# Kernel tuning notes

Measured on AMD Instinct MI355X. Metric: run time of the kernel, lower is better.

The kernel has to match this reference:

```python
import jax, jax.numpy as jnp
import numpy as np

HPC = 42  # HPC_FEATURES_LEN

def setup_inputs() -> dict:
    key = jax.random.key(0)
    ks = jax.random.split(key, 8)
    B, N, C, P, S = 4, 16384, 103, 2048, 32
    xyz = jax.random.normal(ks[0], (B, N, 3), dtype=jnp.float32)
    features = jax.random.normal(ks[1], (B, C, N), dtype=jnp.float32)
    new_xyz = jax.random.normal(ks[2], (B, P, 3), dtype=jnp.float32)
    idx = jax.random.randint(ks[3], (B, P, S), 0, N, dtype=jnp.int32)
    # 1x1-conv weights (out_ch, in_ch); gate conv sees full 3+C=106 channels
    Wg = jax.random.normal(ks[4], (64, 106), dtype=jnp.float32) * 0.05
    bg = jnp.zeros((64,), dtype=jnp.float32)
    W1 = jax.random.normal(ks[5], (64, 64), dtype=jnp.float32) * 0.05
    b1 = jnp.zeros((64,), dtype=jnp.float32)
    W2 = jax.random.normal(ks[6], (128, 64), dtype=jnp.float32) * 0.05
    b2 = jnp.zeros((128,), dtype=jnp.float32)
    W3 = jax.random.normal(ks[7], (256, 128), dtype=jnp.float32) * 0.05
    b3 = jnp.zeros((256,), dtype=jnp.float32)
    return {"xyz": xyz, "features": features, "new_xyz": new_xyz, "idx": idx,
            "Wg": Wg, "bg": bg, "W1": W1, "b1": b1, "W2": W2, "b2": b2,
            "W3": W3, "b3": b3}

def reference(xyz, features, new_xyz, idx, Wg, bg, W1, b1, W2, b2, W3, b3):
    # --- grouping: gather neighbors, center xyz, concat features ---
    # grouped_xyz: (B, P, S, 3) -> (B, 3, P, S)
    grouped_xyz = jax.vmap(lambda x, i: x[i])(xyz, idx) - new_xyz[:, :, None, :]
    grouped_xyz = jnp.transpose(grouped_xyz, (0, 3, 1, 2))
    # grouped_feat: (B, C, P, S)
    grouped_feat = jax.vmap(lambda f, i: f[:, i])(features, idx)
    nf = jnp.concatenate([grouped_xyz, grouped_feat], axis=1)  # (B, 3+C, P, S)
    base = nf[:, :-HPC]                                        # (B, 3+C-42, P, S)
    # --- gating 1x1 conv on full channels, then elementwise gate ---
    w = jnp.einsum('bcps,oc->bops', nf, Wg) + bg[None, :, None, None]
    x = base * (1.0 + w)
    # --- 1x1-conv MLP stack with ReLU ---
    for W, b in ((W1, b1), (W2, b2), (W3, b3)):
        x = jax.nn.relu(jnp.einsum('bcps,oc->bops', x, W) + b[None, :, None, None])
    # --- max pool over nsample ---
    pooled = jnp.max(x, axis=-1)  # (B, 256, P)
    return new_xyz, pooled
```

## Files before the change

kernel.cpp:

```cpp
#include <hip/hip_runtime.h>
#include <stdint.h>


namespace {
constexpr int kB = 4, kN = 16384, kC = 103, kP = 2048, kS = 32;

using short8 = __attribute__((ext_vector_type(8))) short;
using short4 = __attribute__((ext_vector_type(4))) short;
using f32x4  = __attribute__((ext_vector_type(4))) float;

constexpr int WG_HI = 0,     WG_LO = 8192;
constexpr int W1_HI = 16384, W1_LO = 20480;
constexpr int W2_HI = 24576, W2_LO = 32768;
constexpr int W3_HI = 40960, W3_LO = 73728;
constexpr size_t FT_OFF    = 262144;
constexpr size_t FT_SHORTS = (size_t)kB * kN * 128;
constexpr size_t WS_NEED   = FT_OFF + 2 * FT_SHORTS * 2;

__device__ __forceinline__ unsigned short f2bf(float x) {
    unsigned u = __float_as_uint(x);
    u += 0x7fffu + ((u >> 16) & 1u);
    return (unsigned short)(u >> 16);
}
__device__ __forceinline__ float bf2f(unsigned short h) {
    return __uint_as_float((unsigned)h << 16);
}

__global__ void copy_newxyz(const float* __restrict__ src, float* __restrict__ dst, int n) {
    int i = blockIdx.x * blockDim.x + threadIdx.x;
    if (i < n) dst[i] = src[i];
}

__global__ void prep_weights(const float* __restrict__ Wg, const float* __restrict__ W1,
                             const float* __restrict__ W2, const float* __restrict__ W3,
                             short* __restrict__ ws) {
    int i = blockIdx.x * blockDim.x + threadIdx.x;
    if (i >= 53248) return;
    float w; int hi, lo, j;
    if (i < 8192)       { j = i;         int o = j >> 7, c = j & 127; w = (c < 106) ? Wg[o * 106 + c] : 0.f; hi = WG_HI; lo = WG_LO; }
    else if (i < 12288) { j = i - 8192;  int o = j >> 6, c = j & 63;  w = W1[o * 64 + c];  hi = W1_HI; lo = W1_LO; }
    else if (i < 20480) { j = i - 12288; int o = j >> 6, c = j & 63;  w = W2[o * 64 + c];  hi = W2_HI; lo = W2_LO; }
    else                { j = i - 20480; int o = j >> 7, c = j & 127; w = W3[o * 128 + c]; hi = W3_HI; lo = W3_LO; }
    unsigned short h = f2bf(w);
    ws[hi + j] = (short)h;
    ws[lo + j] = (short)f2bf(w - bf2f(h));
}

__global__ __launch_bounds__(512) void prep_feat(const float* __restrict__ f,
                                                 short* __restrict__ ftH, short* __restrict__ ftL) {
    __shared__ float tile[kC][65];
    const int bb = blockIdx.x >> 8;
    const int n0 = (blockIdx.x & 255) * 64;
    const int tid = threadIdx.x;
    for (int c = tid >> 6; c < kC; c += 8)
        tile[c][tid & 63] = f[((size_t)bb * kC + c) * kN + n0 + (tid & 63)];
    __syncthreads();
    const int np = tid >> 3, gc = tid & 7;
    short* rH = ftH + ((size_t)bb * kN + n0 + np) * 128;
    short* rL = ftL + ((size_t)bb * kN + n0 + np) * 128;
    #pragma unroll
    for (int kk = 0; kk < 2; ++kk) {
        const int chunk = gc + 8 * kk;
        union { uint4 u; short s[8]; } H, L;
        #pragma unroll
        for (int e = 0; e < 8; ++e) {
            const int col = chunk * 8 + e;
            float v = (col >= 3 && col < 106) ? tile[col - 3][np] : 0.f;
            unsigned short hh = f2bf(v);
            H.s[e] = (short)hh;
            L.s[e] = (short)f2bf(v - bf2f(hh));
        }
        *(uint4*)(rH + chunk * 8) = H.u;
        *(uint4*)(rL + chunk * 8) = L.u;
    }
}

template<int NOT, int NPT, int KT, int LDC, int LDW, bool INIT>
__device__ __forceinline__ void gemm_core(
    const short* __restrict__ xh, const short* __restrict__ xl,
    const short* __restrict__ wh, const short* __restrict__ wl,
    const float* __restrict__ bias, int kwoff,
    int ot0, int pt0t, int lane, f32x4 (&acc)[NOT][NPT])
{
    const int q = lane >> 4, n16 = lane & 15;
    if constexpr (INIT) {
        #pragma unroll
        for (int i = 0; i < NOT; ++i) {
            const f32x4 binit = *(const f32x4*)(bias + (ot0 + i) * 16 + 4 * q);
            #pragma unroll
            for (int j = 0; j < NPT; ++j) acc[i][j] = binit;
        }
    }
    #pragma unroll
    for (int kt = 0; kt < KT; ++kt) {
        const int k0 = kt * 32 + q * 8;
        short8 bh[NPT], bl[NPT];
        #pragma unroll
        for (int j = 0; j < NPT; ++j) {
            const int p = (pt0t + j) * 16 + n16;
            const int e = p * LDC + (k0 ^ ((p & 7) << 3));
            bh[j] = *(const short8*)(xh + e);
            bl[j] = *(const short8*)(xl + e);
        }
        #pragma unroll
        for (int i = 0; i < NOT; ++i) {
            const size_t we = (size_t)((ot0 + i) * 16 + n16) * LDW + kwoff + k0;
            const short8 ah = *(const short8*)(wh + we);
            const short8 al = *(const short8*)(wl + we);
            #pragma unroll
            for (int j = 0; j < NPT; ++j) {
                acc[i][j] = __builtin_amdgcn_mfma_f32_16x16x32_bf16(ah, bh[j], acc[i][j], 0, 0, 0);
                acc[i][j] = __builtin_amdgcn_mfma_f32_16x16x32_bf16(ah, bl[j], acc[i][j], 0, 0, 0);
                acc[i][j] = __builtin_amdgcn_mfma_f32_16x16x32_bf16(al, bh[j], acc[i][j], 0, 0, 0);
            }
        }
    }
}

template<int NOT, int NPT, bool GATE, int LDCO>
__device__ __forceinline__ void store_act(
    f32x4 (&acc)[NOT][NPT], short* __restrict__ oh, short* __restrict__ ol,
    const short* __restrict__ nfh, const short* __restrict__ nfl,
    int ot0, int pt0t, int lane)
{
    const int q = lane >> 4, n16 = lane & 15;
    #pragma unroll
    for (int i = 0; i < NOT; ++i) {
        const int ob = (ot0 + i) * 16 + 4 * q;
        #pragma unroll
        for (int j = 0; j < NPT; ++j) {
            const int p = (pt0t + j) * 16 + n16;
            const int cs = ob ^ ((p & 7) << 3);
            float v[4];
            #pragma unroll
            for (int r = 0; r < 4; ++r) v[r] = acc[i][j][r];
            if (GATE) {
                const short4 h4 = *(const short4*)(nfh + p * 128 + cs);
                const short4 l4 = *(const short4*)(nfl + p * 128 + cs);
                #pragma unroll
                for (int r = 0; r < 4; ++r) {
                    const float base = bf2f((unsigned short)h4[r]) + bf2f((unsigned short)l4[r]);
                    v[r] = fmaf(base, v[r], base);
                }
            } else {
                #pragma unroll
                for (int r = 0; r < 4; ++r) v[r] = fmaxf(v[r], 0.f);
            }
            short4 h4o, l4o;
            #pragma unroll
            for (int r = 0; r < 4; ++r) {
                const unsigned short h = f2bf(v[r]);
                h4o[r] = (short)h;
                l4o[r] = (short)f2bf(v[r] - bf2f(h));
            }
            *(short4*)(oh + p * LDCO + cs) = h4o;
            *(short4*)(ol + p * LDCO + cs) = l4o;
        }
    }
}

template<bool DENSE>
__global__ __launch_bounds__(512, 3) void pointnet_sa(
    const float* __restrict__ xyz, const float* __restrict__ features,
    const float* __restrict__ new_xyz, const int* __restrict__ idx,
    const short* __restrict__ ws, const short* __restrict__ ftH, const short* __restrict__ ftL,
    const float* __restrict__ bg, const float* __restrict__ b1,
    const float* __restrict__ b2, const float* __restrict__ b3,
    float* __restrict__ out_pooled)
{
    __shared__ alignas(16) short smem[24576];
    short* NFh = smem;
    short* NFl = smem + 8192;
    short* X0h = smem + 16384;
    short* X0l = smem + 20480;

    const int tid = threadIdx.x, lane = tid & 63, wave = tid >> 6;
    const int q = lane >> 4, n16 = lane & 15;
    const int pt0 = blockIdx.x * 64;
    const int b = pt0 >> 16;

    if (DENSE) {
        const int gp = tid >> 3, gc = tid & 7;
        const int pt = pt0 + gp;
        const int n = idx[pt];
        const short* rH = ftH + ((size_t)b * kN + n) * 128;
        const short* rL = ftL + ((size_t)b * kN + n) * 128;
        uint4 hc0 = *(const uint4*)(rH + gc * 8);
        uint4 hc1 = *(const uint4*)(rH + gc * 8 + 64);
        uint4 lc0 = *(const uint4*)(rL + gc * 8);
        uint4 lc1 = *(const uint4*)(rL + gc * 8 + 64);
        if (gc == 0) {
            const float* xp = xyz + ((size_t)b * kN + n) * 3;
            const int pp = (pt >> 5) & (kP - 1);
            const float* np = new_xyz + ((size_t)b * kP + pp) * 3;
            union { uint4 u; short s[8]; } H, L;
            H.u = hc0; L.u = lc0;
            #pragma unroll
            for (int c = 0; c < 3; ++c) {
                const float v = xp[c] - np[c];
                const unsigned short hh = f2bf(v);
                H.s[c] = (short)hh;
                L.s[c] = (short)f2bf(v - bf2f(hh));
            }
            hc0 = H.u; lc0 = L.u;
        }
        const int sw = (gc ^ (gp & 7)) * 8;
        *(uint4*)(NFh + gp * 128 + sw)      = hc0;
        *(uint4*)(NFh + gp * 128 + sw + 64) = hc1;
        *(uint4*)(NFl + gp * 128 + sw)      = lc0;
        *(uint4*)(NFl + gp * 128 + sw + 64) = lc1;
    } else {
        const int p = tid & 63;
        const int cg = tid >> 6;
        const int pt = pt0 + p;
        const int n = idx[pt];
        const int pp = (pt >> 5) & (kP - 1);
        const float* fbp = features + (size_t)b * kC * kN + n;
        const float* xp = xyz + ((size_t)b * kN + n) * 3;
        const float* np = new_xyz + ((size_t)b * kP + pp) * 3;
        for (int c = cg; c < 128; c += 8) {
            float v;
            if (c < 3)        v = xp[c] - np[c];
            else if (c < 106) v = fbp[(size_t)(c - 3) * kN];
            else              v = 0.f;
            const unsigned short h = f2bf(v);
            const int cs = c ^ ((p & 7) << 3);
            NFh[p * 128 + cs] = (short)h;
            NFl[p * 128 + cs] = (short)f2bf(v - bf2f(h));
        }
    }
    __syncthreads();

    {
        f32x4 a[1][2];
        gemm_core<1, 2, 4, 128, 128, true>(NFh, NFl, ws + WG_HI, ws + WG_LO, bg, 0,
                                           wave & 3, 2 * (wave >> 2), lane, a);
        store_act<1, 2, true, 64>(a, X0h, X0l, NFh, NFl, wave & 3, 2 * (wave >> 2), lane);
    }
    __syncthreads();

    {
        f32x4 a[1][2];
        gemm_core<1, 2, 2, 64, 64, true>(X0h, X0l, ws + W1_HI, ws + W1_LO, b1, 0,
                                         wave & 3, 2 * (wave >> 2), lane, a);
        store_act<1, 2, false, 128>(a, NFh, NFl, nullptr, nullptr,
                                    wave & 3, 2 * (wave >> 2), lane);
    }
    __syncthreads();

    {
        f32x4 a[2][2];
        gemm_core<2, 2, 2, 128, 64, true>(NFh, NFl, ws + W2_HI, ws + W2_LO, b2, 0,
                                          2 * (wave & 3), 2 * (wave >> 2), lane, a);
        if ((wave & 3) < 2)
            store_act<2, 2, false, 64>(a, X0h, X0l, nullptr, nullptr,
                                       2 * (wave & 3), 2 * (wave >> 2), lane);
        else
            store_act<2, 2, false, 128>(a, NFh + 64, NFl + 64, nullptr, nullptr,
                                        (2 * (wave & 3)) & 3, 2 * (wave >> 2), lane);
    }
    __syncthreads();

    {
        f32x4 a[2][4];
        gemm_core<2, 4, 2, 64, 128, true >(X0h, X0l, ws + W3_HI, ws + W3_LO, b3, 0,
                                           2 * wave, 0, lane, a);
        gemm_core<2, 4, 2, 128, 128, false>(NFh + 64, NFl + 64, ws + W3_HI, ws + W3_LO,
                                            nullptr, 64, 2 * wave, 0, lane, a);
        #pragma unroll
        for (int i = 0; i < 2; ++i) {
            #pragma unroll
            for (int sg = 0; sg < 2; ++sg) {
                #pragma unroll
                for (int r = 0; r < 4; ++r) {
                    float v = fmaxf(a[i][2 * sg][r], a[i][2 * sg + 1][r]);
                    v = fmaxf(v, __shfl_xor(v, 1, 16));
                    v = fmaxf(v, __shfl_xor(v, 2, 16));
                    v = fmaxf(v, __shfl_xor(v, 4, 16));
                    v = fmaxf(v, __shfl_xor(v, 8, 16));
                    v = fmaxf(v, 0.f);
                    if (n16 == 0) {
                        const int o = (2 * wave + i) * 16 + 4 * q + r;
                        const int g = (pt0 >> 5) + sg;
                        out_pooled[((size_t)(g >> 11) * 256 + o) * kP + (g & (kP - 1))] = v;
                    }
                }
            }
        }
    }
}
}

extern "C" void kernel_launch(void* const* d_in, const int* in_sizes, int n_in,
                              void* d_out, int out_size, void* d_ws, size_t ws_size,
                              hipStream_t stream) {
    const float* xyz      = (const float*)d_in[0];
    const float* features = (const float*)d_in[1];
    const float* new_xyz  = (const float*)d_in[2];
    const int*   idx      = (const int*)d_in[3];
    const float* Wg = (const float*)d_in[4];
    const float* bg = (const float*)d_in[5];
    const float* W1 = (const float*)d_in[6];
    const float* b1 = (const float*)d_in[7];
    const float* W2 = (const float*)d_in[8];
    const float* b2 = (const float*)d_in[9];
    const float* W3 = (const float*)d_in[10];
    const float* b3 = (const float*)d_in[11];
    float* out = (float*)d_out;
    short* ws  = (short*)d_ws;
    short* ftH = (short*)((char*)d_ws + FT_OFF);
    short* ftL = ftH + FT_SHORTS;

    const int nxyz = kB * kP * 3;
    copy_newxyz<<<(nxyz + 255) / 256, 256, 0, stream>>>(new_xyz, out, nxyz);
    prep_weights<<<(53248 + 255) / 256, 256, 0, stream>>>(Wg, W1, W2, W3, ws);

    float* pooled = out + nxyz;
    if (ws_size >= WS_NEED) {
        prep_feat<<<kB * (kN / 64), 512, 0, stream>>>(features, ftH, ftL);
        pointnet_sa<true><<<(kB * kP * kS) / 64, 512, 0, stream>>>(
            xyz, features, new_xyz, idx, ws, ftH, ftL, bg, b1, b2, b3, pooled);
    } else {
        pointnet_sa<false><<<(kB * kP * kS) / 64, 512, 0, stream>>>(
            xyz, features, new_xyz, idx, ws, nullptr, nullptr, bg, b1, b2, b3, pooled);
    }
}
```

Measured before the change: 184.8 us.

## Feed gate GEMM directly from gathered global rows, skip LDS staging of grouped features

The dense path no longer stages gathered feature rows into shared memory. Each lane loads its MFMA B-operand fragments straight from the pre-transposed bf16 hi/lo feature table, and the xyz offsets are patched into the first k-chunk. This removes a 32KB LDS tile and one barrier, which shrinks shared memory to 32KB so more blocks can be resident. The layer-3 input is now written as one contiguous 128-wide buffer, and bf16 hi/lo splitting uses the packed v_cvt_pk_bf16_f32 instruction. In exchange, gathered rows are re-read from global/L2 by several waves instead of once.

```diff
diff --git a/kernel.cpp b/kernel.cpp
--- a/kernel.cpp
+++ b/kernel.cpp
@@ -24,6 +24,21 @@
 }
 __device__ __forceinline__ float bf2f(unsigned short h) {
     return __uint_as_float((unsigned)h << 16);
+}
+__device__ __forceinline__ unsigned cvtpk(float a, float b) {
+    unsigned r;
+    asm("v_cvt_pk_bf16_f32 %0, %1, %2" : "=v"(r) : "v"(a), "v"(b));
+    return r;
+}
+__device__ __forceinline__ void pack4(const float v[4], uint2& H, uint2& L) {
+    H.x = cvtpk(v[0], v[1]);
+    H.y = cvtpk(v[2], v[3]);
+    const float r0 = v[0] - __uint_as_float(H.x << 16);
+    const float r1 = v[1] - __uint_as_float(H.x & 0xffff0000u);
+    const float r2 = v[2] - __uint_as_float(H.y << 16);
+    const float r3 = v[3] - __uint_as_float(H.y & 0xffff0000u);
+    L.x = cvtpk(r0, r1);
+    L.y = cvtpk(r2, r3);
 }
 
 __global__ void copy_newxyz(const float* __restrict__ src, float* __restrict__ dst, int n) {
@@ -75,21 +90,19 @@
     }
 }
 
-template<int NOT, int NPT, int KT, int LDC, int LDW, bool INIT>
-__device__ __forceinline__ void gemm_core(
+template<int NOT, int NPT, int KT, int LDC, int LDW>
+__device__ __forceinline__ void gemm_lds(
     const short* __restrict__ xh, const short* __restrict__ xl,
     const short* __restrict__ wh, const short* __restrict__ wl,
-    const float* __restrict__ bias, int kwoff,
+    const float* __restrict__ bias,
     int ot0, int pt0t, int lane, f32x4 (&acc)[NOT][NPT])
 {
     const int q = lane >> 4, n16 = lane & 15;
-    if constexpr (INIT) {
-        #pragma unroll
-        for (int i = 0; i < NOT; ++i) {
-            const f32x4 binit = *(const f32x4*)(bias + (ot0 + i) * 16 + 4 * q);
-            #pragma unroll
-            for (int j = 0; j < NPT; ++j) acc[i][j] = binit;
-        }
+    #pragma unroll
+    for (int i = 0; i < NOT; ++i) {
+        const f32x4 binit = *(const f32x4*)(bias + (ot0 + i) * 16 + 4 * q);
+        #pragma unroll
+        for (int j = 0; j < NPT; ++j) acc[i][j] = binit;
     }
     #pragma unroll
     for (int kt = 0; kt < KT; ++kt) {
@@ -104,7 +117,7 @@
         }
         #pragma unroll
         for (int i = 0; i < NOT; ++i) {
-            const size_t we = (size_t)((ot0 + i) * 16 + n16) * LDW + kwoff + k0;
+            const size_t we = (size_t)((ot0 + i) * 16 + n16) * LDW + k0;
             const short8 ah = *(const short8*)(wh + we);
             const short8 al = *(const short8*)(wl + we);
             #pragma unroll
@@ -117,10 +130,9 @@
     }
 }
 
-template<int NOT, int NPT, bool GATE, int LDCO>
-__device__ __forceinline__ void store_act(
+template<int NOT, int NPT, int LDCO>
+__device__ __forceinline__ void store_relu(
     f32x4 (&acc)[NOT][NPT], short* __restrict__ oh, short* __restrict__ ol,
-    const short* __restrict__ nfh, const short* __restrict__ nfl,
     int ot0, int pt0t, int lane)
 {
     const int q = lane >> 4, n16 = lane & 15;
@@ -133,37 +145,173 @@
             const int cs = ob ^ ((p & 7) << 3);
             float v[4];
             #pragma unroll
-            for (int r = 0; r < 4; ++r) v[r] = acc[i][j][r];
-            if (GATE) {
-                const short4 h4 = *(const short4*)(nfh + p * 128 + cs);
-                const short4 l4 = *(const short4*)(nfl + p * 128 + cs);
+            for (int r = 0; r < 4; ++r) v[r] = fmaxf(acc[i][j][r], 0.f);
+            uint2 H, L;
+            pack4(v, H, L);
+            *(uint2*)(oh + p * LDCO + cs) = H;
+            *(uint2*)(ol + p * LDCO + cs) = L;
+        }
+    }
+}
+
+__global__ __launch_bounds__(512, 3) void pointnet_sa_direct(
+    const float* __restrict__ xyz, const float* __restrict__ new_xyz,
+    const int* __restrict__ idx,
+    const short* __restrict__ ws, const short* __restrict__ ftH, const short* __restrict__ ftL,
+    const float* __restrict__ bg, const float* __restrict__ b1,
+    const float* __restrict__ b2, const float* __restrict__ b3,
+    float* __restrict__ out_pooled)
+{
+    __shared__ alignas(16) short smem[16384];
+    short* X0h = smem;
+    short* X0l = smem + 4096;
+    short* X1h = smem + 8192;
+    short* X1l = smem + 12288;
+    short* X2h = smem;
+    short* X2l = smem + 8192;
+
+    const int tid = threadIdx.x, lane = tid & 63, wave = tid >> 6;
+    const int q = lane >> 4, n16 = lane & 15;
+    const int pt0 = blockIdx.x * 64;
+    const int b = pt0 >> 16;
+    const size_t fbase = (size_t)b * kN;
+
+    {
+        const int ot = wave & 3, ptp = 2 * (wave >> 2);
+        const int ptA = pt0 + ptp * 16 + n16;
+        const int nA = idx[ptA];
+        const int nB = idx[ptA + 16];
+        const short* fhA = ftH + (fbase + nA) * 128;
+        const short* flA = ftL + (fbase + nA) * 128;
+        const short* fhB = ftH + (fbase + nB) * 128;
+        const short* flB = ftL + (fbase + nB) * 128;
+
+        float xb0[3], xb1[3];
+        unsigned short pxh0[3], pxl0[3], pxh1[3], pxl1[3];
+        if (q == 0) {
+            #pragma unroll
+            for (int j = 0; j < 2; ++j) {
+                const int ptf = ptA + j * 16;
+                const int nj = j ? nB : nA;
+                const int pp = (ptf >> 5) & (kP - 1);
+                const float* xp = xyz + (fbase + nj) * 3;
+                const float* np = new_xyz + ((size_t)b * kP + pp) * 3;
+                #pragma unroll
+                for (int c = 0; c < 3; ++c) {
+                    const float xd = xp[c] - np[c];
+                    const unsigned short h = f2bf(xd);
+                    if (j) { xb1[c] = xd; pxh1[c] = h; pxl1[c] = f2bf(xd - bf2f(h)); }
+                    else   { xb0[c] = xd; pxh0[c] = h; pxl0[c] = f2bf(xd - bf2f(h)); }
+                }
+            }
+        }
+
+        f32x4 acc0, acc1;
+        {
+            const f32x4 binit = *(const f32x4*)(bg + ot * 16 + 4 * q);
+            acc0 = binit; acc1 = binit;
+        }
+        #pragma unroll
+        for (int kt = 0; kt < 4; ++kt) {
+            const int ko = kt * 32 + q * 8;
+            short8 bhA = *(const short8*)(fhA + ko);
+            short8 blA = *(const short8*)(flA + ko);
+            short8 bhB = *(const short8*)(fhB + ko);
+            short8 blB = *(const short8*)(flB + ko);
+            if (kt == 0 && q == 0) {
+                bhA[0] = (short)pxh0[0]; bhA[1] = (short)pxh0[1]; bhA[2] = (short)pxh0[2];
+                blA[0] = (short)pxl0[0]; blA[1] = (short)pxl0[1]; blA[2] = (short)pxl0[2];
+                bhB[0] = (short)pxh1[0]; bhB[1] = (short)pxh1[1]; bhB[2] = (short)pxh1[2];
+                blB[0] = (short)pxl1[0]; blB[1] = (short)pxl1[1]; blB[2] = (short)pxl1[2];
+            }
+            const size_t we = (size_t)(ot * 16 + n16) * 128 + ko;
+            const short8 ah = *(const short8*)(ws + WG_HI + we);
+            const short8 al = *(const short8*)(ws + WG_LO + we);
+            acc0 = __builtin_amdgcn_mfma_f32_16x16x32_bf16(ah, bhA, acc0, 0, 0, 0);
+            acc0 = __builtin_amdgcn_mfma_f32_16x16x32_bf16(ah, blA, acc0, 0, 0, 0);
+            acc0 = __builtin_amdgcn_mfma_f32_16x16x32_bf16(al, bhA, acc0, 0, 0, 0);
+            acc1 = __builtin_amdgcn_mfma_f32_16x16x32_bf16(ah, bhB, acc1, 0, 0, 0);
+            acc1 = __builtin_amdgcn_mfma_f32_16x16x32_bf16(ah, blB, acc1, 0, 0, 0);
+            acc1 = __builtin_amdgcn_mfma_f32_16x16x32_bf16(al, bhB, acc1, 0, 0, 0);
+        }
+
+        const int ob = ot * 16 + 4 * q;
+        #pragma unroll
+        for (int j = 0; j < 2; ++j) {
+            const int pl = (ptp + j) * 16 + n16;
+            const short* fh = j ? fhB : fhA;
+            const short* fl = j ? flB : flA;
+            const uint2 bh4 = *(const uint2*)(fh + ob);
+            const uint2 bl4 = *(const uint2*)(fl + ob);
+            float base[4];
+            base[0] = __uint_as_float(bh4.x << 16)          + __uint_as_float(bl4.x << 16);
+            base[1] = __uint_as_float(bh4.x & 0xffff0000u)  + __uint_as_float(bl4.x & 0xffff0000u);
+            base[2] = __uint_as_float(bh4.y << 16)          + __uint_as_float(bl4.y << 16);
+            base[3] = __uint_as_float(bh4.y & 0xffff0000u)  + __uint_as_float(bl4.y & 0xffff0000u);
+            if (ot == 0 && q == 0) {
+                base[0] = j ? xb1[0] : xb0[0];
+                base[1] = j ? xb1[1] : xb0[1];
+                base[2] = j ? xb1[2] : xb0[2];
+            }
+            const f32x4 A = j ? acc1 : acc0;
+            float v[4];
+            #pragma unroll
+            for (int r = 0; r < 4; ++r) v[r] = fmaf(base[r], A[r], base[r]);
+            uint2 H, L;
+            pack4(v, H, L);
+            const int cs = ob ^ ((pl & 7) << 3);
+            *(uint2*)(X0h + pl * 64 + cs) = H;
+            *(uint2*)(X0l + pl * 64 + cs) = L;
+        }
+    }
+    __syncthreads();
+
+    {
+        f32x4 a[1][2];
+        gemm_lds<1, 2, 2, 64, 64>(X0h, X0l, ws + W1_HI, ws + W1_LO, b1,
+                                  wave & 3, 2 * (wave >> 2), lane, a);
+        store_relu<1, 2, 64>(a, X1h, X1l, wave & 3, 2 * (wave >> 2), lane);
+    }
+    __syncthreads();
+
+    f32x4 a2[2][2];
+    gemm_lds<2, 2, 2, 64, 64>(X1h, X1l, ws + W2_HI, ws + W2_LO, b2,
+                              2 * (wave & 3), 2 * (wave >> 2), lane, a2);
+    __syncthreads();
+    store_relu<2, 2, 128>(a2, X2h, X2l, 2 * (wave & 3), 2 * (wave >> 2), lane);
+    __syncthreads();
+
+    {
+        f32x4 a[2][4];
+        gemm_lds<2, 4, 4, 128, 128>(X2h, X2l, ws + W3_HI, ws + W3_LO, b3,
+                                    2 * wave, 0, lane, a);
+        #pragma unroll
+        for (int i = 0; i < 2; ++i) {
+            #pragma unroll
+            for (int sg = 0; sg < 2; ++sg) {
                 #pragma unroll
                 for (int r = 0; r < 4; ++r) {
-                    const float base = bf2f((unsigned short)h4[r]) + bf2f((unsigned short)l4[r]);
-                    v[r] = fmaf(base, v[r], base);
+                    float v = fmaxf(a[i][2 * sg][r], a[i][2 * sg + 1][r]);
+                    v = fmaxf(v, __shfl_xor(v, 1, 16));
+                    v = fmaxf(v, __shfl_xor(v, 2, 16));
+                    v = fmaxf(v, __shfl_xor(v, 4, 16));
+                    v = fmaxf(v, __shfl_xor(v, 8, 16));
+                    v = fmaxf(v, 0.f);
+                    if (n16 == 0) {
+                        const int o = (2 * wave + i) * 16 + 4 * q + r;
+                        const int g = (pt0 >> 5) + sg;
+                        out_pooled[((size_t)(g >> 11) * 256 + o) * kP + (g & (kP - 1))] = v;
+                    }
                 }
-            } else {
-                #pragma unroll
-                for (int r = 0; r < 4; ++r) v[r] = fmaxf(v[r], 0.f);
-            }
-            short4 h4o, l4o;
-            #pragma unroll
-            for (int r = 0; r < 4; ++r) {
-                const unsigned short h = f2bf(v[r]);
-                h4o[r] = (short)h;
-                l4o[r] = (short)f2bf(v[r] - bf2f(h));
-            }
-            *(short4*)(oh + p * LDCO + cs) = h4o;
-            *(short4*)(ol + p * LDCO + cs) = l4o;
-        }
-    }
-}
-
-template<bool DENSE>
-__global__ __launch_bounds__(512, 3) void pointnet_sa(
+            }
+        }
+    }
+}
+
+__global__ __launch_bounds__(512, 2) void pointnet_sa_scalar(
     const float* __restrict__ xyz, const float* __restrict__ features,
     const float* __restrict__ new_xyz, const int* __restrict__ idx,
-    const short* __restrict__ ws, const short* __restrict__ ftH, const short* __restrict__ ftL,
+    const short* __restrict__ ws,
     const float* __restrict__ bg, const float* __restrict__ b1,
     const float* __restrict__ b2, const float* __restrict__ b3,
     float* __restrict__ out_pooled)
@@ -179,37 +327,7 @@
     const int pt0 = blockIdx.x * 64;
     const int b = pt0 >> 16;
 
-    if (DENSE) {
-        const int gp = tid >> 3, gc = tid & 7;
-        const int pt = pt0 + gp;
-        const int n = idx[pt];
-        const short* rH = ftH + ((size_t)b * kN + n) * 128;
-        const short* rL = ftL + ((size_t)b * kN + n) * 128;
-        uint4 hc0 = *(const uint4*)(rH + gc * 8);
-        uint4 hc1 = *(const uint4*)(rH + gc * 8 + 64);
-        uint4 lc0 = *(const uint4*)(rL + gc * 8);
-        uint4 lc1 = *(const uint4*)(rL + gc * 8 + 64);
-        if (gc == 0) {
-            const float* xp = xyz + ((size_t)b * kN + n) * 3;
-            const int pp = (pt >> 5) & (kP - 1);
-            const float* np = new_xyz + ((size_t)b * kP + pp) * 3;
-            union { uint4 u; short s[8]; } H, L;
-            H.u = hc0; L.u = lc0;
-            #pragma unroll
-            for (int c = 0; c < 3; ++c) {
-                const float v = xp[c] - np[c];
-                const unsigned short hh = f2bf(v);
-                H.s[c] = (short)hh;
-                L.s[c] = (short)f2bf(v - bf2f(hh));
-            }
-            hc0 = H.u; lc0 = L.u;
-        }
-        const int sw = (gc ^ (gp & 7)) * 8;
-        *(uint4*)(NFh + gp * 128 + sw)      = hc0;
-        *(uint4*)(NFh + gp * 128 + sw + 64) = hc1;
-        *(uint4*)(NFl + gp * 128 + sw)      = lc0;
-        *(uint4*)(NFl + gp * 128 + sw + 64) = lc1;
-    } else {
+    {
         const int p = tid & 63;
         const int cg = tid >> 6;
         const int pt = pt0 + p;
@@ -230,47 +348,85 @@
         }
     }
     __syncthreads();
-
     {
         f32x4 a[1][2];
-        gemm_core<1, 2, 4, 128, 128, true>(NFh, NFl, ws + WG_HI, ws + WG_LO, bg, 0,
-                                           wave & 3, 2 * (wave >> 2), lane, a);
-        store_act<1, 2, true, 64>(a, X0h, X0l, NFh, NFl, wave & 3, 2 * (wave >> 2), lane);
-    }
-    __syncthreads();
-
+        gemm_lds<1, 2, 4, 128, 128>(NFh, NFl, ws + WG_HI, ws + WG_LO, bg,
+                                    wave & 3, 2 * (wave >> 2), lane, a);
+        const int ot0 = wave & 3, ptp = 2 * (wave >> 2);
+        const int ob = ot0 * 16 + 4 * q;
+        #pragma unroll
+        for (int j = 0; j < 2; ++j) {
+            const int p = (ptp + j) * 16 + n16;
+            const int cs = ob ^ ((p & 7) << 3);
+            const short4 h4 = *(const short4*)(NFh + p * 128 + cs);
+            const short4 l4 = *(const short4*)(NFl + p * 128 + cs);
+            float v[4];
+            #pragma unroll
+            for (int r = 0; r < 4; ++r) {
+                const float base = bf2f((unsigned short)h4[r]) + bf2f((unsigned short)l4[r]);
+                v[r] = fmaf(base, a[0][j][r], base);
+            }
+            uint2 H, L;
+            pack4(v, H, L);
+            *(uint2*)(X0h + p * 64 + cs) = H;
+            *(uint2*)(X0l + p * 64 + cs) = L;
+        }
+    }
+    __syncthreads();
     {
         f32x4 a[1][2];
-        gemm_core<1, 2, 2, 64, 64, true>(X0h, X0l, ws + W1_HI, ws + W1_LO, b1, 0,
-                                         wave & 3, 2 * (wave >> 2), lane, a);
-        store_act<1, 2, false, 128>(a, NFh, NFl, nullptr, nullptr,
-                                    wave & 3, 2 * (wave >> 2), lane);
-    }
-    __syncthreads();
-
+        gemm_lds<1, 2, 2, 64, 64>(X0h, X0l, ws + W1_HI, ws + W1_LO, b1,
+                                  wave & 3, 2 * (wave >> 2), lane, a);
+        store_relu<1, 2, 128>(a, NFh, NFl, wave & 3, 2 * (wave >> 2), lane);
+    }
+    __syncthreads();
     {
         f32x4 a[2][2];
-        gemm_core<2, 2, 2, 128, 64, true>(NFh, NFl, ws + W2_HI, ws + W2_LO, b2, 0,
-                                          2 * (wave & 3), 2 * (wave >> 2), lane, a);
+        gemm_lds<2, 2, 2, 128, 64>(NFh, NFl, ws + W2_HI, ws + W2_LO, b2,
+                                   2 * (wave & 3), 2 * (wave >> 2), lane, a);
+        __syncthreads();
         if ((wave & 3) < 2)
-            store_act<2, 2, false, 64>(a, X0h, X0l, nullptr, nullptr,
-                                       2 * (wave & 3), 2 * (wave >> 2), lane);
+            store_relu<2, 2, 64>(a, X0h, X0l, 2 * (wave & 3), 2 * (wave >> 2), lane);
         else
-            store_act<2, 2, false, 128>(a, NFh + 64, NFl + 64, nullptr, nullptr,
-                                        (2 * (wave & 3)) & 3, 2 * (wave >> 2), lane);
-    }
-    __syncthreads();
-
+            store_relu<2, 2, 128>(a, NFh + 64, NFl + 64, (2 * (wave & 3)) & 3,
+                                  2 * (wave >> 2), lane);
+    }
+    __syncthreads();
     {
         f32x4 a[2][4];
-        gemm_core<2, 4, 2, 64, 128, true >(X0h, X0l, ws + W3_HI, ws + W3_LO, b3, 0,
-                                           2 * wave, 0, lane, a);
-        gemm_core<2, 4, 2, 128, 128, false>(NFh + 64, NFl + 64, ws + W3_HI, ws + W3_LO,
-                                            nullptr, 64, 2 * wave, 0, lane, a);
-        #pragma unroll
-        for (int i = 0; i < 2; ++i) {
-            #pragma unroll
-            for (int sg = 0; sg < 2; ++sg) {
+        gemm_lds<2, 4, 2, 64, 128>(X0h, X0l, ws + W3_HI, ws + W3_LO, b3,
+                                   2 * wave, 0, lane, a);
+        {
+            const int q2 = lane >> 4, nn = lane & 15;
+            #pragma unroll
+            for (int kt = 0; kt < 2; ++kt) {
+                const int k0 = kt * 32 + q2 * 8;
+                short8 bh[4], bl[4];
+                #pragma unroll
+                for (int j = 0; j < 4; ++j) {
+                    const int p = j * 16 + nn;
+                    const int e = p * 128 + (k0 ^ ((p & 7) << 3));
+                    bh[j] = *(const short8*)(NFh + 64 + e);
+                    bl[j] = *(const short8*)(NFl + 64 + e);
+                }
+                #pragma unroll
+                for (int i = 0; i < 2; ++i) {
+                    const size_t we = (size_t)((2 * wave + i) * 16 + nn) * 128 + 64 + k0;
+                    const short8 ah = *(const short8*)(ws + W3_HI + we);
+                    const short8 al = *(const short8*)(ws + W3_LO + we);
+                    #pragma unroll
+                    for (int j = 0; j < 4; ++j) {
+                        a[i][j] = __builtin_amdgcn_mfma_f32_16x16x32_bf16(ah, bh[j], a[i][j], 0, 0, 0);
+                        a[i][j] = __builtin_amdgcn_mfma_f32_16x16x32_bf16(ah, bl[j], a[i][j], 0, 0, 0);
+                        a[i][j] = __builtin_amdgcn_mfma_f32_16x16x32_bf16(al, bh[j], a[i][j], 0, 0, 0);
+                    }
+                }
+            }
+        }
+        #pragma unroll
+        for (int i = 0; i < 2; ++i)
+            #pragma unroll
+            for (int sg = 0; sg < 2; ++sg)
                 #pragma unroll
                 for (int r = 0; r < 4; ++r) {
                     float v = fmaxf(a[i][2 * sg][r], a[i][2 * sg + 1][r]);
@@ -285,8 +441,6 @@
                         out_pooled[((size_t)(g >> 11) * 256 + o) * kP + (g & (kP - 1))] = v;
                     }
                 }
-            }
-        }
     }
 }
 }
@@ -318,10 +472,10 @@
     float* pooled = out + nxyz;
     if (ws_size >= WS_NEED) {
         prep_feat<<<kB * (kN / 64), 512, 0, stream>>>(features, ftH, ftL);
-        pointnet_sa<true><<<(kB * kP * kS) / 64, 512, 0, stream>>>(
-            xyz, features, new_xyz, idx, ws, ftH, ftL, bg, b1, b2, b3, pooled);
+        pointnet_sa_direct<<<(kB * kP * kS) / 64, 512, 0, stream>>>(
+            xyz, new_xyz, idx, ws, ftH, ftL, bg, b1, b2, b3, pooled);
     } else {
-        pointnet_sa<false><<<(kB * kP * kS) / 64, 512, 0, stream>>>(
-            xyz, features, new_xyz, idx, ws, nullptr, nullptr, bg, b1, b2, b3, pooled);
-    }
-}
+        pointnet_sa_scalar<<<(kB * kP * kS) / 64, 512, 0, stream>>>(
+            xyz, features, new_xyz, idx, ws, bg, b1, b2, b3, pooled);
+    }
+}
```

New measurement: 246.0 us. +33.1%, slower.

## Shrink dense workgroup to one sample group and pack bf16 via cvt_pk

Applied to the files above, without the earlier changes.

The dense path now processes 32 points (one nsample group) per 256-thread block with half the shared memory and launch bounds of 6 blocks per CU, redistributing the per-wave output tiles. This is meant to raise occupancy and shorten per-block barrier chains. It also replaces the manual bf16 hi/lo rounding with the hardware v_cvt_pk_bf16_f32 packed conversion to cut ALU work in the activation store. The scalar fallback is split into its own kernel, and the launch_bounds change adds some risk of register spilling.

```diff
diff --git a/kernel.cpp b/kernel.cpp
--- a/kernel.cpp
+++ b/kernel.cpp
@@ -24,6 +24,21 @@
 }
 __device__ __forceinline__ float bf2f(unsigned short h) {
     return __uint_as_float((unsigned)h << 16);
+}
+__device__ __forceinline__ unsigned cvtpk(float a, float b) {
+    unsigned r;
+    asm("v_cvt_pk_bf16_f32 %0, %1, %2" : "=v"(r) : "v"(a), "v"(b));
+    return r;
+}
+__device__ __forceinline__ void pack4(const float v[4], uint2& H, uint2& L) {
+    H.x = cvtpk(v[0], v[1]);
+    H.y = cvtpk(v[2], v[3]);
+    const float r0 = v[0] - __uint_as_float(H.x << 16);
+    const float r1 = v[1] - __uint_as_float(H.x & 0xffff0000u);
+    const float r2 = v[2] - __uint_as_float(H.y << 16);
+    const float r3 = v[3] - __uint_as_float(H.y & 0xffff0000u);
+    L.x = cvtpk(r0, r1);
+    L.y = cvtpk(r2, r3);
 }
 
 __global__ void copy_newxyz(const float* __restrict__ src, float* __restrict__ dst, int n) {
@@ -132,65 +147,58 @@
             const int p = (pt0t + j) * 16 + n16;
             const int cs = ob ^ ((p & 7) << 3);
             float v[4];
-            #pragma unroll
-            for (int r = 0; r < 4; ++r) v[r] = acc[i][j][r];
             if (GATE) {
                 const short4 h4 = *(const short4*)(nfh + p * 128 + cs);
                 const short4 l4 = *(const short4*)(nfl + p * 128 + cs);
                 #pragma unroll
                 for (int r = 0; r < 4; ++r) {
                     const float base = bf2f((unsigned short)h4[r]) + bf2f((unsigned short)l4[r]);
-                    v[r] = fmaf(base, v[r], base);
+                    v[r] = fmaf(base, acc[i][j][r], base);
                 }
             } else {
                 #pragma unroll
-                for (int r = 0; r < 4; ++r) v[r] = fmaxf(v[r], 0.f);
+                for (int r = 0; r < 4; ++r) v[r] = fmaxf(acc[i][j][r], 0.f);
             }
-            short4 h4o, l4o;
-            #pragma unroll
-            for (int r = 0; r < 4; ++r) {
-                const unsigned short h = f2bf(v[r]);
-                h4o[r] = (short)h;
-                l4o[r] = (short)f2bf(v[r] - bf2f(h));
-            }
-            *(short4*)(oh + p * LDCO + cs) = h4o;
-            *(short4*)(ol + p * LDCO + cs) = l4o;
-        }
-    }
-}
-
-template<bool DENSE>
-__global__ __launch_bounds__(512, 3) void pointnet_sa(
-    const float* __restrict__ xyz, const float* __restrict__ features,
-    const float* __restrict__ new_xyz, const int* __restrict__ idx,
+            uint2 H, L;
+            pack4(v, H, L);
+            *(uint2*)(oh + p * LDCO + cs) = H;
+            *(uint2*)(ol + p * LDCO + cs) = L;
+        }
+    }
+}
+
+__global__ __launch_bounds__(256, 6) void pointnet_sa(
+    const float* __restrict__ xyz, const float* __restrict__ new_xyz,
+    const int* __restrict__ idx,
     const short* __restrict__ ws, const short* __restrict__ ftH, const short* __restrict__ ftL,
     const float* __restrict__ bg, const float* __restrict__ b1,
     const float* __restrict__ b2, const float* __restrict__ b3,
     float* __restrict__ out_pooled)
 {
-    __shared__ alignas(16) short smem[24576];
+    __shared__ alignas(16) short smem[12288];
     short* NFh = smem;
-    short* NFl = smem + 8192;
-    short* X0h = smem + 16384;
-    short* X0l = smem + 20480;
+    short* NFl = smem + 4096;
+    short* X0h = smem + 8192;
+    short* X0l = smem + 10240;
 
     const int tid = threadIdx.x, lane = tid & 63, wave = tid >> 6;
     const int q = lane >> 4, n16 = lane & 15;
-    const int pt0 = blockIdx.x * 64;
+    const int pt0 = blockIdx.x * 32;
     const int b = pt0 >> 16;
-
-    if (DENSE) {
+    const size_t fbase = (size_t)b * kN;
+
+    {
         const int gp = tid >> 3, gc = tid & 7;
         const int pt = pt0 + gp;
         const int n = idx[pt];
-        const short* rH = ftH + ((size_t)b * kN + n) * 128;
-        const short* rL = ftL + ((size_t)b * kN + n) * 128;
+        const short* rH = ftH + (fbase + n) * 128;
+        const short* rL = ftL + (fbase + n) * 128;
         uint4 hc0 = *(const uint4*)(rH + gc * 8);
         uint4 hc1 = *(const uint4*)(rH + gc * 8 + 64);
         uint4 lc0 = *(const uint4*)(rL + gc * 8);
         uint4 lc1 = *(const uint4*)(rL + gc * 8 + 64);
         if (gc == 0) {
-            const float* xp = xyz + ((size_t)b * kN + n) * 3;
+            const float* xp = xyz + (fbase + n) * 3;
             const int pp = (pt >> 5) & (kP - 1);
             const float* np = new_xyz + ((size_t)b * kP + pp) * 3;
             union { uint4 u; short s[8]; } H, L;
@@ -209,7 +217,84 @@
         *(uint4*)(NFh + gp * 128 + sw + 64) = hc1;
         *(uint4*)(NFl + gp * 128 + sw)      = lc0;
         *(uint4*)(NFl + gp * 128 + sw + 64) = lc1;
-    } else {
+    }
+    __syncthreads();
+
+    {
+        f32x4 a[1][2];
+        gemm_core<1, 2, 4, 128, 128, true>(NFh, NFl, ws + WG_HI, ws + WG_LO, bg, 0,
+                                           wave, 0, lane, a);
+        store_act<1, 2, true, 64>(a, X0h, X0l, NFh, NFl, wave, 0, lane);
+    }
+    __syncthreads();
+
+    {
+        f32x4 a[1][2];
+        gemm_core<1, 2, 2, 64, 64, true>(X0h, X0l, ws + W1_HI, ws + W1_LO, b1, 0,
+                                         wave, 0, lane, a);
+        store_act<1, 2, false, 128>(a, NFh, NFl, nullptr, nullptr, wave, 0, lane);
+    }
+    __syncthreads();
+
+    {
+        f32x4 a[2][2];
+        gemm_core<2, 2, 2, 128, 64, true>(NFh, NFl, ws + W2_HI, ws + W2_LO, b2, 0,
+                                          2 * wave, 0, lane, a);
+        if (wave < 2)
+            store_act<2, 2, false, 64>(a, X0h, X0l, nullptr, nullptr, 2 * wave, 0, lane);
+        else
+            store_act<2, 2, false, 128>(a, NFh + 64, NFl + 64, nullptr, nullptr,
+                                        2 * wave - 4, 0, lane);
+    }
+    __syncthreads();
+
+    {
+        f32x4 a[4][2];
+        gemm_core<4, 2, 2, 64, 128, true >(X0h, X0l, ws + W3_HI, ws + W3_LO, b3, 0,
+                                           4 * wave, 0, lane, a);
+        gemm_core<4, 2, 2, 128, 128, false>(NFh + 64, NFl + 64, ws + W3_HI, ws + W3_LO,
+                                            nullptr, 64, 4 * wave, 0, lane, a);
+        const int g = blockIdx.x;
+        float* outp = out_pooled + ((size_t)(g >> 11) * 256) * kP + (g & (kP - 1));
+        #pragma unroll
+        for (int i = 0; i < 4; ++i) {
+            #pragma unroll
+            for (int r = 0; r < 4; ++r) {
+                float v = fmaxf(a[i][0][r], a[i][1][r]);
+                v = fmaxf(v, __shfl_xor(v, 1, 16));
+                v = fmaxf(v, __shfl_xor(v, 2, 16));
+                v = fmaxf(v, __shfl_xor(v, 4, 16));
+                v = fmaxf(v, __shfl_xor(v, 8, 16));
+                v = fmaxf(v, 0.f);
+                if (n16 == 0) {
+                    const int o = (4 * wave + i) * 16 + 4 * q + r;
+                    outp[(size_t)o * kP] = v;
+                }
+            }
+        }
+    }
+}
+
+__global__ __launch_bounds__(512, 2) void pointnet_sa_scalar(
+    const float* __restrict__ xyz, const float* __restrict__ features,
+    const float* __restrict__ new_xyz, const int* __restrict__ idx,
+    const short* __restrict__ ws,
+    const float* __restrict__ bg, const float* __restrict__ b1,
+    const float* __restrict__ b2, const float* __restrict__ b3,
+    float* __restrict__ out_pooled)
+{
+    __shared__ alignas(16) short smem[24576];
+    short* NFh = smem;
+    short* NFl = smem + 8192;
+    short* X0h = smem + 16384;
+    short* X0l = smem + 20480;
+
+    const int tid = threadIdx.x, lane = tid & 63, wave = tid >> 6;
+    const int q = lane >> 4, n16 = lane & 15;
+    const int pt0 = blockIdx.x * 64;
+    const int b = pt0 >> 16;
+
+    {
         const int p = tid & 63;
         const int cg = tid >> 6;
         const int pt = pt0 + p;
@@ -230,7 +315,6 @@
         }
     }
     __syncthreads();
-
     {
         f32x4 a[1][2];
         gemm_core<1, 2, 4, 128, 128, true>(NFh, NFl, ws + WG_HI, ws + WG_LO, bg, 0,
@@ -238,7 +322,6 @@
         store_act<1, 2, true, 64>(a, X0h, X0l, NFh, NFl, wave & 3, 2 * (wave >> 2), lane);
     }
     __syncthreads();
-
     {
         f32x4 a[1][2];
         gemm_core<1, 2, 2, 64, 64, true>(X0h, X0l, ws + W1_HI, ws + W1_LO, b1, 0,
@@ -247,7 +330,6 @@
                                     wave & 3, 2 * (wave >> 2), lane);
     }
     __syncthreads();
-
     {
         f32x4 a[2][2];
         gemm_core<2, 2, 2, 128, 64, true>(NFh, NFl, ws + W2_HI, ws + W2_LO, b2, 0,
@@ -260,7 +342,6 @@
                                         (2 * (wave & 3)) & 3, 2 * (wave >> 2), lane);
     }
     __syncthreads();
-
     {
         f32x4 a[2][4];
         gemm_core<2, 4, 2, 64, 128, true >(X0h, X0l, ws + W3_HI, ws + W3_LO, b3, 0,
@@ -268,9 +349,9 @@
         gemm_core<2, 4, 2, 128, 128, false>(NFh + 64, NFl + 64, ws + W3_HI, ws + W3_LO,
                                             nullptr, 64, 2 * wave, 0, lane, a);
         #pragma unroll
-        for (int i = 0; i < 2; ++i) {
+        for (int i = 0; i < 2; ++i)
             #pragma unroll
-            for (int sg = 0; sg < 2; ++sg) {
+            for (int sg = 0; sg < 2; ++sg)
                 #pragma unroll
                 for (int r = 0; r < 4; ++r) {
                     float v = fmaxf(a[i][2 * sg][r], a[i][2 * sg + 1][r]);
@@ -285,8 +366,6 @@
                         out_pooled[((size_t)(g >> 11) * 256 + o) * kP + (g & (kP - 1))] = v;
                     }
                 }
-            }
-        }
     }
 }
 }
@@ -318,10 +397,10 @@
     float* pooled = out + nxyz;
     if (ws_size >= WS_NEED) {
         prep_feat<<<kB * (kN / 64), 512, 0, stream>>>(features, ftH, ftL);
-        pointnet_sa<true><<<(kB * kP * kS) / 64, 512, 0, stream>>>(
-            xyz, features, new_xyz, idx, ws, ftH, ftL, bg, b1, b2, b3, pooled);
+        pointnet_sa<<<(kB * kP * kS) / 32, 256, 0, stream>>>(
+            xyz, new_xyz, idx, ws, ftH, ftL, bg, b1, b2, b3, pooled);
     } else {
-        pointnet_sa<false><<<(kB * kP * kS) / 64, 512, 0, stream>>>(
-            xyz, features, new_xyz, idx, ws, nullptr, nullptr, bg, b1, b2, b3, pooled);
-    }
-}
+        pointnet_sa_scalar<<<(kB * kP * kS) / 64, 512, 0, stream>>>(
+            xyz, features, new_xyz, idx, ws, bg, b1, b2, b3, pooled);
+    }
+}
```

After: 227.8 us. +23.3%, slower.

## Hoist weight fragments into registers, use packed bf16 convert, relax occupancy bound

Applied to the files above, without the earlier changes.

Weight A-fragments (hi and lo) for all K tiles are preloaded into registers once per gemm_core call instead of reloaded inside the K loop. Activation stores now use the hardware v_cvt_pk_bf16_f32 instruction to pack pairs into hi/lo bf16 words, replacing the software round-to-nearest-even conversion. The launch bound drops from 3 to 2 blocks per CU so the extra weight registers fit without spilling, at the cost of fewer resident waves to hide latency.

```diff
diff --git a/kernel.cpp b/kernel.cpp
--- a/kernel.cpp
+++ b/kernel.cpp
@@ -24,6 +24,21 @@
 }
 __device__ __forceinline__ float bf2f(unsigned short h) {
     return __uint_as_float((unsigned)h << 16);
+}
+__device__ __forceinline__ unsigned cvtpk(float a, float b) {
+    unsigned r;
+    asm("v_cvt_pk_bf16_f32 %0, %1, %2" : "=v"(r) : "v"(a), "v"(b));
+    return r;
+}
+__device__ __forceinline__ void pack4(const float v[4], uint2& H, uint2& L) {
+    H.x = cvtpk(v[0], v[1]);
+    H.y = cvtpk(v[2], v[3]);
+    const float r0 = v[0] - __uint_as_float(H.x << 16);
+    const float r1 = v[1] - __uint_as_float(H.x & 0xffff0000u);
+    const float r2 = v[2] - __uint_as_float(H.y << 16);
+    const float r3 = v[3] - __uint_as_float(H.y & 0xffff0000u);
+    L.x = cvtpk(r0, r1);
+    L.y = cvtpk(r2, r3);
 }
 
 __global__ void copy_newxyz(const float* __restrict__ src, float* __restrict__ dst, int n) {
@@ -83,6 +98,15 @@
     int ot0, int pt0t, int lane, f32x4 (&acc)[NOT][NPT])
 {
     const int q = lane >> 4, n16 = lane & 15;
+    short8 whr[NOT * KT], wlr[NOT * KT];
+    #pragma unroll
+    for (int i = 0; i < NOT; ++i)
+        #pragma unroll
+        for (int kt = 0; kt < KT; ++kt) {
+            const size_t we = (size_t)((ot0 + i) * 16 + n16) * LDW + kwoff + kt * 32 + q * 8;
+            whr[i * KT + kt] = *(const short8*)(wh + we);
+            wlr[i * KT + kt] = *(const short8*)(wl + we);
+        }
     if constexpr (INIT) {
         #pragma unroll
         for (int i = 0; i < NOT; ++i) {
@@ -104,9 +128,8 @@
         }
         #pragma unroll
         for (int i = 0; i < NOT; ++i) {
-            const size_t we = (size_t)((ot0 + i) * 16 + n16) * LDW + kwoff + k0;
-            const short8 ah = *(const short8*)(wh + we);
-            const short8 al = *(const short8*)(wl + we);
+            const short8 ah = whr[i * KT + kt];
+            const short8 al = wlr[i * KT + kt];
             #pragma unroll
             for (int j = 0; j < NPT; ++j) {
                 acc[i][j] = __builtin_amdgcn_mfma_f32_16x16x32_bf16(ah, bh[j], acc[i][j], 0, 0, 0);
@@ -132,35 +155,28 @@
             const int p = (pt0t + j) * 16 + n16;
             const int cs = ob ^ ((p & 7) << 3);
             float v[4];
-            #pragma unroll
-            for (int r = 0; r < 4; ++r) v[r] = acc[i][j][r];
             if (GATE) {
                 const short4 h4 = *(const short4*)(nfh + p * 128 + cs);
                 const short4 l4 = *(const short4*)(nfl + p * 128 + cs);
                 #pragma unroll
                 for (int r = 0; r < 4; ++r) {
                     const float base = bf2f((unsigned short)h4[r]) + bf2f((unsigned short)l4[r]);
-                    v[r] = fmaf(base, v[r], base);
+                    v[r] = fmaf(base, acc[i][j][r], base);
                 }
             } else {
                 #pragma unroll
-                for (int r = 0; r < 4; ++r) v[r] = fmaxf(v[r], 0.f);
+                for (int r = 0; r < 4; ++r) v[r] = fmaxf(acc[i][j][r], 0.f);
             }
-            short4 h4o, l4o;
-            #pragma unroll
-            for (int r = 0; r < 4; ++r) {
-                const unsigned short h = f2bf(v[r]);
-                h4o[r] = (short)h;
-                l4o[r] = (short)f2bf(v[r] - bf2f(h));
-            }
-            *(short4*)(oh + p * LDCO + cs) = h4o;
-            *(short4*)(ol + p * LDCO + cs) = l4o;
+            uint2 H, L;
+            pack4(v, H, L);
+            *(uint2*)(oh + p * LDCO + cs) = H;
+            *(uint2*)(ol + p * LDCO + cs) = L;
         }
     }
 }
 
 template<bool DENSE>
-__global__ __launch_bounds__(512, 3) void pointnet_sa(
+__global__ __launch_bounds__(512, 2) void pointnet_sa(
     const float* __restrict__ xyz, const float* __restrict__ features,
     const float* __restrict__ new_xyz, const int* __restrict__ idx,
     const short* __restrict__ ws, const short* __restrict__ ftH, const short* __restrict__ ftL,
```

After: 183.2 us. About the same (-0.9%).
